# Optimization experiments

Hardware: AMD Instinct MI355X
Metric: run time of the kernel (lower is better)

## Reference

```python
import jax, jax.numpy as jnp
import numpy as np

N, M, D = 1024, 1024, 512


def setup_inputs() -> dict:
    key = jax.random.key(0)
    ks = jax.random.split(key, 12)
    s = 1.0 / np.sqrt(D)
    return {
        "q": jax.random.normal(ks[0], (N, D), jnp.float32),
        "k": jax.random.normal(ks[1], (M, D), jnp.float32),
        "v": jax.random.normal(ks[2], (M, D), jnp.float32),
        "mask": jax.random.randint(ks[3], (N, M), 0, 2) > 0,
        "Wq": jax.random.normal(ks[4], (D, D), jnp.float32) * s,
        "bq": jax.random.normal(ks[5], (D,), jnp.float32) * s,
        "Wk": jax.random.normal(ks[6], (D, D), jnp.float32) * s,
        "bk": jax.random.normal(ks[7], (D,), jnp.float32) * s,
        "Wv": jax.random.normal(ks[8], (D, D), jnp.float32) * s,
        "bv": jax.random.normal(ks[9], (D,), jnp.float32) * s,
        "Ww": jax.random.normal(ks[10], (D,), jnp.float32) * s,
        "bw": jax.random.normal(ks[11], (1,), jnp.float32) * s,
    }


def reference(q, k, v, mask, Wq, bq, Wk, bk, Wv, bv, Ww, bw):
    # Linear projections (torch Linear: x @ W.T + b)
    qp = q @ Wq.T + bq  # [N, D]
    kp = k @ Wk.T + bk  # [M, D]
    vp = v @ Wv.T + bv  # [M, D]
    # Bahdanau additive score: W(tanh(q_n + k_m)) -> [N, M]
    h = jnp.tanh(qp[:, None, :] + kp[None, :, :])  # [N, M, D]
    scores = jnp.einsum('nmd,d->nm', h, Ww) + bw[0]
    scores = jnp.where(mask, scores, jnp.float32(-1000000.0))
    attn = jax.nn.softmax(scores, axis=1)  # softmax over M (dim 1)
    context = jnp.einsum('nm,md->nd', attn, vp)  # [N, D]
    return context
```

## Files before the change

kernel.cpp:

```cpp
#include <hip/hip_runtime.h>
#include <hip/hip_bf16.h>
#include <float.h>


#define NROWS 1024
#define DDIM  512
#define MDIM  1024

typedef __attribute__((ext_vector_type(8))) short s8v;
typedef __attribute__((ext_vector_type(4))) float f4v;
typedef __attribute__((ext_vector_type(2))) float v2f;

__device__ __forceinline__ ushort f2bf(float f) {
    unsigned u = __float_as_uint(f);
    u = u + 0x7FFFu + ((u >> 16) & 1u);
    return (ushort)(u >> 16);
}
__device__ __forceinline__ float bf2f(ushort h) {
    return __uint_as_float(((unsigned)h) << 16);
}

__device__ __forceinline__ void load_lds16(const float* g, float* l) {
    __builtin_amdgcn_global_load_lds(
        (const __attribute__((address_space(1))) void*)g,
        (__attribute__((address_space(3))) void*)l, 16, 0, 0);
}

__global__ __launch_bounds__(256) void proj_gemm(
    const float* __restrict__ q, const float* __restrict__ kk_,
    const float* __restrict__ v,
    const float* __restrict__ Wq, const float* __restrict__ bq,
    const float* __restrict__ Wk, const float* __restrict__ bk,
    const float* __restrict__ Wv, const float* __restrict__ bv,
    float* __restrict__ eq, float* __restrict__ ekT,
    ushort* __restrict__ vph, ushort* __restrict__ vpl,
    float* __restrict__ S, float CS)
{
    __shared__ ushort Ah[4096], Al[4096], Bh[4096], Bl[4096];

    const float* A; const float* B; const float* bias;
    int biasRow;
    if (blockIdx.z == 0)      { A = q;   B = Wq;  bias = bq; biasRow = 0; }
    else if (blockIdx.z == 1) { A = Wk;  B = kk_; bias = bk; biasRow = 1; }
    else                      { A = Wv;  B = v;   bias = bv; biasRow = 1; }

    const int bi = (blockIdx.z == 0) ? blockIdx.x : blockIdx.y;
    const int bj = (blockIdx.z == 0) ? blockIdx.y : blockIdx.x;

    const int t    = threadIdx.x;
    const int lane = t & 63;
    const int w    = t >> 6;
    const int lm   = lane & 15;
    const int lq   = lane >> 4;
    const int i0   = bi * 64;
    const int j0   = bj * 64;
    const int mh   = (w >> 1) * 32;
    const int nh   = (w & 1) * 32;

    if (blockIdx.z == 0) {
        const int jb = blockIdx.x * 8 + blockIdx.y;
        float4 zz = {0.f, 0.f, 0.f, 0.f};
#pragma unroll
        for (int p = 0; p < 8; ++p)
            *(float4*)&S[(size_t)jb * 8192 + (t + p * 256) * 4] = zz;
    }

    f4v acc[2][2] = {{{0.f,0.f,0.f,0.f},{0.f,0.f,0.f,0.f}},
                     {{0.f,0.f,0.f,0.f},{0.f,0.f,0.f,0.f}}};
    float4 pa[4], pb[4];

    const int sr = t >> 4, sc4 = t & 15;
#pragma unroll
    for (int p = 0; p < 4; ++p) {
        int r = sr + p * 16;
        pa[p] = *(const float4*)&A[(size_t)(i0 + r) * DDIM + sc4 * 4];
        pb[p] = *(const float4*)&B[(size_t)(j0 + r) * DDIM + sc4 * 4];
    }

    for (int kc = 0; kc < 8; ++kc) {
        __syncthreads();
#pragma unroll
        for (int p = 0; p < 4; ++p) {
            int r = sr + p * 16;
            int ad = r * 64 + (((sc4 >> 1) ^ (r & 7)) << 3) + (sc4 & 1) * 4;
            float af[4] = {pa[p].x, pa[p].y, pa[p].z, pa[p].w};
            float bf[4] = {pb[p].x, pb[p].y, pb[p].z, pb[p].w};
            ushort ah4[4], al4[4], bh4[4], bl4[4];
#pragma unroll
            for (int e = 0; e < 4; ++e) {
                ah4[e] = f2bf(af[e]); al4[e] = f2bf(af[e] - bf2f(ah4[e]));
                bh4[e] = f2bf(bf[e]); bl4[e] = f2bf(bf[e] - bf2f(bh4[e]));
            }
            *(ushort4*)&Ah[ad] = *(ushort4*)ah4;
            *(ushort4*)&Al[ad] = *(ushort4*)al4;
            *(ushort4*)&Bh[ad] = *(ushort4*)bh4;
            *(ushort4*)&Bl[ad] = *(ushort4*)bl4;
        }
        __syncthreads();
        if (kc < 7) {
            const int k0 = (kc + 1) * 64;
#pragma unroll
            for (int p = 0; p < 4; ++p) {
                int r = sr + p * 16;
                pa[p] = *(const float4*)&A[(size_t)(i0 + r) * DDIM + k0 + sc4 * 4];
                pb[p] = *(const float4*)&B[(size_t)(j0 + r) * DDIM + k0 + sc4 * 4];
            }
        }
#pragma unroll
        for (int ks = 0; ks < 2; ++ks) {
            const int kb = ks * 4 + lq;
            s8v afh[2], afl[2], bfh[2], bfl[2];
#pragma unroll
            for (int g = 0; g < 2; ++g) {
                int ra = mh + g * 16 + lm;
                int rb = nh + g * 16 + lm;
                int aa = ra * 64 + ((kb ^ (ra & 7)) << 3);
                int ab = rb * 64 + ((kb ^ (rb & 7)) << 3);
                afh[g] = *(const s8v*)&Ah[aa];
                afl[g] = *(const s8v*)&Al[aa];
                bfh[g] = *(const s8v*)&Bh[ab];
                bfl[g] = *(const s8v*)&Bl[ab];
            }
#pragma unroll
            for (int mi = 0; mi < 2; ++mi)
#pragma unroll
                for (int ni = 0; ni < 2; ++ni) {
                    acc[mi][ni] = __builtin_amdgcn_mfma_f32_16x16x32_bf16(
                        afh[mi], bfh[ni], acc[mi][ni], 0, 0, 0);
                    acc[mi][ni] = __builtin_amdgcn_mfma_f32_16x16x32_bf16(
                        afh[mi], bfl[ni], acc[mi][ni], 0, 0, 0);
                    acc[mi][ni] = __builtin_amdgcn_mfma_f32_16x16x32_bf16(
                        afl[mi], bfh[ni], acc[mi][ni], 0, 0, 0);
                }
        }
    }

    const float CLAMP = 8192.0f;
#pragma unroll
    for (int mi = 0; mi < 2; ++mi) {
#pragma unroll
        for (int ni = 0; ni < 2; ++ni) {
#pragma unroll
            for (int p = 0; p < 4; ++p) {
                int row = i0 + mh + mi * 16 + lq * 4 + p;
                int col = j0 + nh + ni * 16 + lm;
                float val = acc[mi][ni][p] + (biasRow ? bias[row] : bias[col]);
                if (blockIdx.z == 0) {
                    eq[(size_t)row * 512 + col] =
                        fminf(__builtin_amdgcn_exp2f(val * CS), CLAMP);
                } else if (blockIdx.z == 1) {
                    ekT[(size_t)row * 1024 + col] =
                        fminf(__builtin_amdgcn_exp2f(val * CS), CLAMP);
                } else {
                    ushort h = f2bf(val);
                    vph[(size_t)row * 1024 + col] = h;
                    vpl[(size_t)row * 1024 + col] = f2bf(val - bf2f(h));
                }
            }
        }
    }
}

#define DCH  32
#define SMCH 128
__global__ __launch_bounds__(256) void score_kernel(const float* __restrict__ eq,
                                                    const float* __restrict__ ekT,
                                                    const float* __restrict__ Ww,
                                                    float* __restrict__ S)
{
    __shared__ __align__(16) float ks[DCH * SMCH];
    __shared__ __align__(16) float es[16 * DCH];
    __shared__ __align__(16) float wws[DCH];
    const int t    = threadIdx.x;
    const int lane = t & 63;
    const int w    = t >> 6;
    const int m0   = blockIdx.x * SMCH;
    const int n0   = blockIdx.y * 16;
    const int dbase = blockIdx.z * 256;

    v2f acc[4] = {};
    const v2f one2 = {1.f, 1.f};

    for (int dc = 0; dc < 256; dc += DCH) {
        const int d0 = dbase + dc;
        __syncthreads();
#pragma unroll
        for (int i = 0; i < 4; ++i) {
            int r2 = w * 8 + i * 2;
            const float* g = ekT + (size_t)(d0 + r2 + (lane >> 5)) * MDIM
                             + m0 + (lane & 31) * 4;
            load_lds16(g, &ks[r2 * SMCH]);
        }
#pragma unroll
        for (int p = 0; p < 2; ++p) {
            int idx = t + p * 256;
            int nl = idx >> 5, dd = idx & 31;
            es[nl * DCH + dd] = eq[(size_t)(n0 + nl) * DDIM + d0 + dd];
        }
        if (t < DCH) wws[t] = Ww[d0 + t];
        __syncthreads();

#pragma unroll
        for (int dq = 0; dq < DCH; dq += 4) {
            v2f k0 = *(const v2f*)&ks[(dq + 0) * SMCH + lane * 2];
            v2f k1 = *(const v2f*)&ks[(dq + 1) * SMCH + lane * 2];
            v2f k2 = *(const v2f*)&ks[(dq + 2) * SMCH + lane * 2];
            v2f k3 = *(const v2f*)&ks[(dq + 3) * SMCH + lane * 2];
            float4 wg = *(const float4*)&wws[dq];
#pragma unroll
            for (int nn = 0; nn < 4; ++nn) {
                float4 eg = *(const float4*)&es[(w * 4 + nn) * DCH + dq];
                v2f A0 = __builtin_elementwise_fma(k0, (v2f){eg.x, eg.x}, one2);
                v2f A1 = __builtin_elementwise_fma(k1, (v2f){eg.y, eg.y}, one2);
                v2f A2 = __builtin_elementwise_fma(k2, (v2f){eg.z, eg.z}, one2);
                v2f A3 = __builtin_elementwise_fma(k3, (v2f){eg.w, eg.w}, one2);
                v2f n01 = __builtin_elementwise_fma((v2f){wg.y, wg.y}, A0,
                                                    (v2f){wg.x, wg.x} * A1);
                v2f d01 = A0 * A1;
                v2f n23 = __builtin_elementwise_fma((v2f){wg.w, wg.w}, A2,
                                                    (v2f){wg.z, wg.z} * A3);
                v2f d23 = A2 * A3;
                v2f num = __builtin_elementwise_fma(n01, d23, n23 * d01);
                v2f den = d01 * d23;
                v2f r = {__builtin_amdgcn_rcpf(den.x), __builtin_amdgcn_rcpf(den.y)};
                acc[nn] = __builtin_elementwise_fma(num, r, acc[nn]);
            }
        }
    }

    const float C2 = -2.8853900817779268f;
    const int m = m0 + lane * 2;
#pragma unroll
    for (int nn = 0; nn < 4; ++nn) {
        int n = n0 + w * 4 + nn;
        atomicAdd(&S[(size_t)n * MDIM + m],     acc[nn].x * C2);
        atomicAdd(&S[(size_t)n * MDIM + m + 1], acc[nn].y * C2);
    }
}

__global__ __launch_bounds__(256) void combine_kernel(const float* __restrict__ S,
                                                      const int* __restrict__ mask,
                                                      ushort* __restrict__ Ph,
                                                      ushort* __restrict__ Pl,
                                                      float* __restrict__ rsum)
{
    __shared__ float red[4];
    const int n = blockIdx.x, t = threadIdx.x;
    const int lane = t & 63, w = t >> 6;

    float4 s  = *(const float4*)&S[(size_t)n * MDIM + t * 4];
    int4   mk = *(const int4*)&mask[(size_t)n * MDIM + t * 4];
    float p0 = mk.x ? __builtin_amdgcn_exp2f(s.x) : 0.f;
    float p1 = mk.y ? __builtin_amdgcn_exp2f(s.y) : 0.f;
    float p2 = mk.z ? __builtin_amdgcn_exp2f(s.z) : 0.f;
    float p3 = mk.w ? __builtin_amdgcn_exp2f(s.w) : 0.f;

    ushort h[4] = {f2bf(p0), f2bf(p1), f2bf(p2), f2bf(p3)};
    ushort l[4] = {f2bf(p0 - bf2f(h[0])), f2bf(p1 - bf2f(h[1])),
                   f2bf(p2 - bf2f(h[2])), f2bf(p3 - bf2f(h[3]))};
    *(ushort4*)&Ph[(size_t)n * MDIM + t * 4] = *(ushort4*)h;
    *(ushort4*)&Pl[(size_t)n * MDIM + t * 4] = *(ushort4*)l;

    float rs = (p0 + p1) + (p2 + p3);
#pragma unroll
    for (int off = 32; off; off >>= 1) rs += __shfl_xor(rs, off);
    if (lane == 0) red[w] = rs;
    __syncthreads();
    if (t == 0) rsum[n] = (red[0] + red[1]) + (red[2] + red[3]);
}

__global__ __launch_bounds__(256) void ctx_gemm(const ushort* __restrict__ Ph,
                                                const ushort* __restrict__ Pl,
                                                const ushort* __restrict__ vph,
                                                const ushort* __restrict__ vpl,
                                                const float* __restrict__ rsum,
                                                float* __restrict__ out)
{
    const int t    = threadIdx.x;
    const int lane = t & 63;
    const int w    = t >> 6;
    const int lm   = lane & 15;
    const int lq   = lane >> 4;
    const int d0   = blockIdx.x * 64 + w * 16;
    const int n0   = blockIdx.y * 16;

    const ushort* pAh = Ph  + (size_t)(n0 + lm) * MDIM + lq * 8;
    const ushort* pAl = Pl  + (size_t)(n0 + lm) * MDIM + lq * 8;
    const ushort* pBh = vph + (size_t)(d0 + lm) * MDIM + lq * 8;
    const ushort* pBl = vpl + (size_t)(d0 + lm) * MDIM + lq * 8;

    f4v acc = {0.f, 0.f, 0.f, 0.f};
#pragma unroll 4
    for (int m0 = 0; m0 < MDIM; m0 += 32) {
        s8v ah = *(const s8v*)(pAh + m0);
        s8v al = *(const s8v*)(pAl + m0);
        s8v bh = *(const s8v*)(pBh + m0);
        s8v bl = *(const s8v*)(pBl + m0);
        acc = __builtin_amdgcn_mfma_f32_16x16x32_bf16(ah, bh, acc, 0, 0, 0);
        acc = __builtin_amdgcn_mfma_f32_16x16x32_bf16(ah, bl, acc, 0, 0, 0);
        acc = __builtin_amdgcn_mfma_f32_16x16x32_bf16(al, bh, acc, 0, 0, 0);
    }

#pragma unroll
    for (int p = 0; p < 4; ++p) {
        int nrow = n0 + lq * 4 + p;
        float inv = __builtin_amdgcn_rcpf(rsum[nrow]);
        out[(size_t)nrow * DDIM + d0 + lm] = acc[p] * inv;
    }
}

extern "C" void kernel_launch(void* const* d_in, const int* in_sizes, int n_in,
                              void* d_out, int out_size, void* d_ws, size_t ws_size,
                              hipStream_t stream)
{
    const float* q    = (const float*)d_in[0];
    const float* k    = (const float*)d_in[1];
    const float* v    = (const float*)d_in[2];
    const int*   mask = (const int*)d_in[3];
    const float* Wq   = (const float*)d_in[4];
    const float* bq   = (const float*)d_in[5];
    const float* Wk   = (const float*)d_in[6];
    const float* bk   = (const float*)d_in[7];
    const float* Wv   = (const float*)d_in[8];
    const float* bv   = (const float*)d_in[9];
    const float* Ww   = (const float*)d_in[10];

    float* ws    = (float*)d_ws;
    float* eq    = ws;
    float* ekT   = ws + 524288;
    ushort* vph  = (ushort*)(ws + 1048576);
    ushort* vpl  = (ushort*)(ws + 1310720);
    float* S     = ws + 1572864;
    float* rsum  = ws + 2621440;
    ushort* Ph   = (ushort*)ws;
    ushort* Pl   = (ushort*)(ws + 524288);
    float* out   = (float*)d_out;

    const float CS = 2.8853900817779268f;

    proj_gemm<<<dim3(16, 8, 3), dim3(256), 0, stream>>>(q, k, v, Wq, bq, Wk, bk,
                                                        Wv, bv, eq, ekT,
                                                        vph, vpl, S, CS);
    score_kernel<<<dim3(8, 64, 2), dim3(256), 0, stream>>>(eq, ekT, Ww, S);
    combine_kernel<<<dim3(1024), dim3(256), 0, stream>>>(S, mask, Ph, Pl, rsum);
    ctx_gemm<<<dim3(8, 64), dim3(256), 0, stream>>>(Ph, Pl, vph, vpl, rsum, out);
}
```

Baseline: 181.4 us.

## Widen score tiles, split-K context GEMM, and use packed bf16 conversions

The score kernel now gives each lane four m columns instead of two and preloads the whole 256-wide eq and Ww slice into LDS once. This halves the blocks along m and removes the per-chunk eq reloads. ctx_gemm is split along M into two halves that atomically add into an output zeroed by proj_gemm, which doubles the grid for occupancy at the cost of extra atomics. Manual bf16 rounding is replaced with packed __float22bfloat162_rn conversions to cut integer ALU work in the projection, combine and split paths.

```diff
diff --git a/kernel.cpp b/kernel.cpp
--- a/kernel.cpp
+++ b/kernel.cpp
@@ -11,13 +11,17 @@
 typedef __attribute__((ext_vector_type(4))) float f4v;
 typedef __attribute__((ext_vector_type(2))) float v2f;
 
-__device__ __forceinline__ ushort f2bf(float f) {
-    unsigned u = __float_as_uint(f);
-    u = u + 0x7FFFu + ((u >> 16) & 1u);
-    return (ushort)(u >> 16);
-}
 __device__ __forceinline__ float bf2f(ushort h) {
     return __uint_as_float(((unsigned)h) << 16);
+}
+__device__ __forceinline__ ushort2 f2bf2(float a, float b) {
+    __hip_bfloat162 t = __float22bfloat162_rn(float2{a, b});
+    union { __hip_bfloat162 v; ushort2 u; } c; c.v = t;
+    return c.u;
+}
+__device__ __forceinline__ void hl2(float a, float b, ushort2& h, ushort2& l) {
+    h = f2bf2(a, b);
+    l = f2bf2(a - bf2f(h.x), b - bf2f(h.y));
 }
 
 __device__ __forceinline__ void load_lds16(const float* g, float* l) {
@@ -34,7 +38,7 @@
     const float* __restrict__ Wv, const float* __restrict__ bv,
     float* __restrict__ eq, float* __restrict__ ekT,
     ushort* __restrict__ vph, ushort* __restrict__ vpl,
-    float* __restrict__ S, float CS)
+    float* __restrict__ S, float* __restrict__ outz, float CS)
 {
     __shared__ ushort Ah[4096], Al[4096], Bh[4096], Bl[4096];
 
@@ -58,11 +62,17 @@
     const int nh   = (w & 1) * 32;
 
     if (blockIdx.z == 0) {
-        const int jb = blockIdx.x * 8 + blockIdx.y;
+        const int flat = blockIdx.x * 8 + blockIdx.y;
         float4 zz = {0.f, 0.f, 0.f, 0.f};
 #pragma unroll
         for (int p = 0; p < 8; ++p)
-            *(float4*)&S[(size_t)jb * 8192 + (t + p * 256) * 4] = zz;
+            *(float4*)&S[(size_t)flat * 8192 + (t + p * 256) * 4] = zz;
+    } else if (blockIdx.z == 2) {
+        const int flat = blockIdx.x * 8 + blockIdx.y;
+        float4 zz = {0.f, 0.f, 0.f, 0.f};
+#pragma unroll
+        for (int p = 0; p < 4; ++p)
+            *(float4*)&outz[(size_t)flat * 4096 + (t + p * 256) * 4] = zz;
     }
 
     f4v acc[2][2] = {{{0.f,0.f,0.f,0.f},{0.f,0.f,0.f,0.f}},
@@ -83,18 +93,19 @@
         for (int p = 0; p < 4; ++p) {
             int r = sr + p * 16;
             int ad = r * 64 + (((sc4 >> 1) ^ (r & 7)) << 3) + (sc4 & 1) * 4;
-            float af[4] = {pa[p].x, pa[p].y, pa[p].z, pa[p].w};
-            float bf[4] = {pb[p].x, pb[p].y, pb[p].z, pb[p].w};
-            ushort ah4[4], al4[4], bh4[4], bl4[4];
-#pragma unroll
-            for (int e = 0; e < 4; ++e) {
-                ah4[e] = f2bf(af[e]); al4[e] = f2bf(af[e] - bf2f(ah4[e]));
-                bh4[e] = f2bf(bf[e]); bl4[e] = f2bf(bf[e] - bf2f(bh4[e]));
-            }
-            *(ushort4*)&Ah[ad] = *(ushort4*)ah4;
-            *(ushort4*)&Al[ad] = *(ushort4*)al4;
-            *(ushort4*)&Bh[ad] = *(ushort4*)bh4;
-            *(ushort4*)&Bl[ad] = *(ushort4*)bl4;
+            ushort2 h01, l01, h23, l23;
+            hl2(pa[p].x, pa[p].y, h01, l01);
+            hl2(pa[p].z, pa[p].w, h23, l23);
+            ushort4 ha = {h01.x, h01.y, h23.x, h23.y};
+            ushort4 la = {l01.x, l01.y, l23.x, l23.y};
+            *(ushort4*)&Ah[ad] = ha;
+            *(ushort4*)&Al[ad] = la;
+            hl2(pb[p].x, pb[p].y, h01, l01);
+            hl2(pb[p].z, pb[p].w, h23, l23);
+            ushort4 hb = {h01.x, h01.y, h23.x, h23.y};
+            ushort4 lb = {l01.x, l01.y, l23.x, l23.y};
+            *(ushort4*)&Bh[ad] = hb;
+            *(ushort4*)&Bl[ad] = lb;
         }
         __syncthreads();
         if (kc < 7) {
@@ -152,9 +163,10 @@
                     ekT[(size_t)row * 1024 + col] =
                         fminf(__builtin_amdgcn_exp2f(val * CS), CLAMP);
                 } else {
-                    ushort h = f2bf(val);
-                    vph[(size_t)row * 1024 + col] = h;
-                    vpl[(size_t)row * 1024 + col] = f2bf(val - bf2f(h));
+                    ushort2 h2 = f2bf2(val, val);
+                    vph[(size_t)row * 1024 + col] = h2.x;
+                    ushort2 l2 = f2bf2(val - bf2f(h2.x), 0.f);
+                    vpl[(size_t)row * 1024 + col] = l2.x;
                 }
             }
         }
@@ -162,15 +174,15 @@
 }
 
 #define DCH  32
-#define SMCH 128
+#define SMCH 256
 __global__ __launch_bounds__(256) void score_kernel(const float* __restrict__ eq,
                                                     const float* __restrict__ ekT,
                                                     const float* __restrict__ Ww,
                                                     float* __restrict__ S)
 {
     __shared__ __align__(16) float ks[DCH * SMCH];
-    __shared__ __align__(16) float es[16 * DCH];
-    __shared__ __align__(16) float wws[DCH];
+    __shared__ __align__(16) float es[16 * 256];
+    __shared__ __align__(16) float wws[256];
     const int t    = threadIdx.x;
     const int lane = t & 63;
     const int w    = t >> 6;
@@ -178,63 +190,73 @@
     const int n0   = blockIdx.y * 16;
     const int dbase = blockIdx.z * 256;
 
-    v2f acc[4] = {};
+#pragma unroll
+    for (int p = 0; p < 4; ++p) {
+        int idx = t + p * 256;
+        int nl = idx >> 6, dd4 = idx & 63;
+        *(float4*)&es[nl * 256 + dd4 * 4] =
+            *(const float4*)&eq[(size_t)(n0 + nl) * DDIM + dbase + dd4 * 4];
+    }
+    wws[t] = Ww[dbase + t];
+
+    v2f acc[4][2] = {};
     const v2f one2 = {1.f, 1.f};
 
     for (int dc = 0; dc < 256; dc += DCH) {
         const int d0 = dbase + dc;
         __syncthreads();
 #pragma unroll
-        for (int i = 0; i < 4; ++i) {
-            int r2 = w * 8 + i * 2;
-            const float* g = ekT + (size_t)(d0 + r2 + (lane >> 5)) * MDIM
-                             + m0 + (lane & 31) * 4;
-            load_lds16(g, &ks[r2 * SMCH]);
-        }
-#pragma unroll
-        for (int p = 0; p < 2; ++p) {
-            int idx = t + p * 256;
-            int nl = idx >> 5, dd = idx & 31;
-            es[nl * DCH + dd] = eq[(size_t)(n0 + nl) * DDIM + d0 + dd];
-        }
-        if (t < DCH) wws[t] = Ww[d0 + t];
+        for (int i = 0; i < 8; ++i) {
+            int r = w * 8 + i;
+            load_lds16(ekT + (size_t)(d0 + r) * MDIM + m0 + lane * 4,
+                       &ks[r * SMCH]);
+        }
         __syncthreads();
 
 #pragma unroll
         for (int dq = 0; dq < DCH; dq += 4) {
-            v2f k0 = *(const v2f*)&ks[(dq + 0) * SMCH + lane * 2];
-            v2f k1 = *(const v2f*)&ks[(dq + 1) * SMCH + lane * 2];
-            v2f k2 = *(const v2f*)&ks[(dq + 2) * SMCH + lane * 2];
-            v2f k3 = *(const v2f*)&ks[(dq + 3) * SMCH + lane * 2];
-            float4 wg = *(const float4*)&wws[dq];
+            float4 k0 = *(const float4*)&ks[(dq + 0) * SMCH + lane * 4];
+            float4 k1 = *(const float4*)&ks[(dq + 1) * SMCH + lane * 4];
+            float4 k2 = *(const float4*)&ks[(dq + 2) * SMCH + lane * 4];
+            float4 k3 = *(const float4*)&ks[(dq + 3) * SMCH + lane * 4];
+            float4 wg = *(const float4*)&wws[dc + dq];
+            v2f k0p[2] = {{k0.x, k0.y}, {k0.z, k0.w}};
+            v2f k1p[2] = {{k1.x, k1.y}, {k1.z, k1.w}};
+            v2f k2p[2] = {{k2.x, k2.y}, {k2.z, k2.w}};
+            v2f k3p[2] = {{k3.x, k3.y}, {k3.z, k3.w}};
 #pragma unroll
             for (int nn = 0; nn < 4; ++nn) {
-                float4 eg = *(const float4*)&es[(w * 4 + nn) * DCH + dq];
-                v2f A0 = __builtin_elementwise_fma(k0, (v2f){eg.x, eg.x}, one2);
-                v2f A1 = __builtin_elementwise_fma(k1, (v2f){eg.y, eg.y}, one2);
-                v2f A2 = __builtin_elementwise_fma(k2, (v2f){eg.z, eg.z}, one2);
-                v2f A3 = __builtin_elementwise_fma(k3, (v2f){eg.w, eg.w}, one2);
-                v2f n01 = __builtin_elementwise_fma((v2f){wg.y, wg.y}, A0,
-                                                    (v2f){wg.x, wg.x} * A1);
-                v2f d01 = A0 * A1;
-                v2f n23 = __builtin_elementwise_fma((v2f){wg.w, wg.w}, A2,
-                                                    (v2f){wg.z, wg.z} * A3);
-                v2f d23 = A2 * A3;
-                v2f num = __builtin_elementwise_fma(n01, d23, n23 * d01);
-                v2f den = d01 * d23;
-                v2f r = {__builtin_amdgcn_rcpf(den.x), __builtin_amdgcn_rcpf(den.y)};
-                acc[nn] = __builtin_elementwise_fma(num, r, acc[nn]);
+                float4 eg = *(const float4*)&es[(w * 4 + nn) * 256 + dc + dq];
+#pragma unroll
+                for (int h = 0; h < 2; ++h) {
+                    v2f A0 = __builtin_elementwise_fma(k0p[h], (v2f){eg.x, eg.x}, one2);
+                    v2f A1 = __builtin_elementwise_fma(k1p[h], (v2f){eg.y, eg.y}, one2);
+                    v2f A2 = __builtin_elementwise_fma(k2p[h], (v2f){eg.z, eg.z}, one2);
+                    v2f A3 = __builtin_elementwise_fma(k3p[h], (v2f){eg.w, eg.w}, one2);
+                    v2f n01 = __builtin_elementwise_fma((v2f){wg.y, wg.y}, A0,
+                                                        (v2f){wg.x, wg.x} * A1);
+                    v2f d01 = A0 * A1;
+                    v2f n23 = __builtin_elementwise_fma((v2f){wg.w, wg.w}, A2,
+                                                        (v2f){wg.z, wg.z} * A3);
+                    v2f d23 = A2 * A3;
+                    v2f num = __builtin_elementwise_fma(n01, d23, n23 * d01);
+                    v2f den = d01 * d23;
+                    v2f r = {__builtin_amdgcn_rcpf(den.x), __builtin_amdgcn_rcpf(den.y)};
+                    acc[nn][h] = __builtin_elementwise_fma(num, r, acc[nn][h]);
+                }
             }
         }
     }
 
     const float C2 = -2.8853900817779268f;
-    const int m = m0 + lane * 2;
+    const int m = m0 + lane * 4;
 #pragma unroll
     for (int nn = 0; nn < 4; ++nn) {
         int n = n0 + w * 4 + nn;
-        atomicAdd(&S[(size_t)n * MDIM + m],     acc[nn].x * C2);
-        atomicAdd(&S[(size_t)n * MDIM + m + 1], acc[nn].y * C2);
+        atomicAdd(&S[(size_t)n * MDIM + m + 0], acc[nn][0].x * C2);
+        atomicAdd(&S[(size_t)n * MDIM + m + 1], acc[nn][0].y * C2);
+        atomicAdd(&S[(size_t)n * MDIM + m + 2], acc[nn][1].x * C2);
+        atomicAdd(&S[(size_t)n * MDIM + m + 3], acc[nn][1].y * C2);
     }
 }
 
@@ -255,11 +277,13 @@
     float p2 = mk.z ? __builtin_amdgcn_exp2f(s.z) : 0.f;
     float p3 = mk.w ? __builtin_amdgcn_exp2f(s.w) : 0.f;
 
-    ushort h[4] = {f2bf(p0), f2bf(p1), f2bf(p2), f2bf(p3)};
-    ushort l[4] = {f2bf(p0 - bf2f(h[0])), f2bf(p1 - bf2f(h[1])),
-                   f2bf(p2 - bf2f(h[2])), f2bf(p3 - bf2f(h[3]))};
-    *(ushort4*)&Ph[(size_t)n * MDIM + t * 4] = *(ushort4*)h;
-    *(ushort4*)&Pl[(size_t)n * MDIM + t * 4] = *(ushort4*)l;
+    ushort2 h01, l01, h23, l23;
+    hl2(p0, p1, h01, l01);
+    hl2(p2, p3, h23, l23);
+    ushort4 hv = {h01.x, h01.y, h23.x, h23.y};
+    ushort4 lv = {l01.x, l01.y, l23.x, l23.y};
+    *(ushort4*)&Ph[(size_t)n * MDIM + t * 4] = hv;
+    *(ushort4*)&Pl[(size_t)n * MDIM + t * 4] = lv;
 
     float rs = (p0 + p1) + (p2 + p3);
 #pragma unroll
@@ -283,15 +307,16 @@
     const int lq   = lane >> 4;
     const int d0   = blockIdx.x * 64 + w * 16;
     const int n0   = blockIdx.y * 16;
-
-    const ushort* pAh = Ph  + (size_t)(n0 + lm) * MDIM + lq * 8;
-    const ushort* pAl = Pl  + (size_t)(n0 + lm) * MDIM + lq * 8;
-    const ushort* pBh = vph + (size_t)(d0 + lm) * MDIM + lq * 8;
-    const ushort* pBl = vpl + (size_t)(d0 + lm) * MDIM + lq * 8;
+    const int mb   = blockIdx.z * 512;
+
+    const ushort* pAh = Ph  + (size_t)(n0 + lm) * MDIM + mb + lq * 8;
+    const ushort* pAl = Pl  + (size_t)(n0 + lm) * MDIM + mb + lq * 8;
+    const ushort* pBh = vph + (size_t)(d0 + lm) * MDIM + mb + lq * 8;
+    const ushort* pBl = vpl + (size_t)(d0 + lm) * MDIM + mb + lq * 8;
 
     f4v acc = {0.f, 0.f, 0.f, 0.f};
 #pragma unroll 4
-    for (int m0 = 0; m0 < MDIM; m0 += 32) {
+    for (int m0 = 0; m0 < 512; m0 += 32) {
         s8v ah = *(const s8v*)(pAh + m0);
         s8v al = *(const s8v*)(pAl + m0);
         s8v bh = *(const s8v*)(pBh + m0);
@@ -305,7 +330,7 @@
     for (int p = 0; p < 4; ++p) {
         int nrow = n0 + lq * 4 + p;
         float inv = __builtin_amdgcn_rcpf(rsum[nrow]);
-        out[(size_t)nrow * DDIM + d0 + lm] = acc[p] * inv;
+        atomicAdd(&out[(size_t)nrow * DDIM + d0 + lm], acc[p] * inv);
     }
 }
 
@@ -340,8 +365,8 @@
 
     proj_gemm<<<dim3(16, 8, 3), dim3(256), 0, stream>>>(q, k, v, Wq, bq, Wk, bk,
                                                         Wv, bv, eq, ekT,
-                                                        vph, vpl, S, CS);
-    score_kernel<<<dim3(8, 64, 2), dim3(256), 0, stream>>>(eq, ekT, Ww, S);
+                                                        vph, vpl, S, out, CS);
+    score_kernel<<<dim3(4, 64, 2), dim3(256), 0, stream>>>(eq, ekT, Ww, S);
     combine_kernel<<<dim3(1024), dim3(256), 0, stream>>>(S, mask, Ph, Pl, rsum);
-    ctx_gemm<<<dim3(8, 64), dim3(256), 0, stream>>>(Ph, Pl, vph, vpl, rsum, out);
-}
+    ctx_gemm<<<dim3(8, 64, 2), dim3(256), 0, stream>>>(Ph, Pl, vph, vpl, rsum, out);
+}
```

Result: slower. 195.4 us (+7.7%).
